# Optimization experiments

Hardware: AMD Instinct MI355X
Metric: run time of the kernel (lower is better)

## Reference

```python
import jax, jax.numpy as jnp
import numpy as np

E, H = 512, 8
D = E // H  # head_dim = 64
NEG = jnp.finfo(jnp.float32).min


def setup_inputs() -> dict:
    key = jax.random.key(0)
    ks = jax.random.split(key, 12)
    s = 0.02
    return {
        "image": jax.random.normal(ks[0], (16, 197, E), jnp.float32),
        "text": jax.random.normal(ks[1], (64, 30, E), jnp.float32),
        "text_mask": jax.random.randint(ks[2], (64, 29), 0, 2).astype(bool),
        "Wq": jax.random.normal(ks[3], (D, D), jnp.float32) * s,
        "Wk": jax.random.normal(ks[4], (D, D), jnp.float32) * s,
        "Wv": jax.random.normal(ks[5], (D, D), jnp.float32) * s,
        "W_out": jax.random.normal(ks[6], (E, E), jnp.float32) * s,
        "b_out": jnp.zeros((E,), jnp.float32),
        "Wtv": jax.random.normal(ks[7], (D, D), jnp.float32) * s,
        "W_out_text": jax.random.normal(ks[8], (E, E), jnp.float32) * s,
        "b_out_text": jnp.zeros((E,), jnp.float32),
    }


def reference(image, text, text_mask, Wq, Wk, Wv, W_out, b_out, Wtv, W_out_text, b_out_text):
    I, Q, _ = image.shape
    T, K, _ = text.shape
    img = image.reshape(I, Q, H, D)
    txt = text.reshape(T, K, H, D)
    # per-head linear projections (torch Linear: y = x @ W.T)
    q = img @ Wq.T            # [I,Q,H,D]
    k = txt @ Wk.T            # [T,K,H,D]
    v = txt @ Wv.T            # [T,K,H,D]
    # cross-batch bidirectional attention energy [I,T,H,Q,K]
    energy = jnp.einsum('tkhd,iqhd->ithqk', k, q)
    # cls_present: pad mask with True at front along K
    mask = jnp.pad(text_mask, ((0, 0), (1, 0)), constant_values=True)  # [T,K]
    energy = jnp.where(mask[None, :, None, None, :], energy, NEG)
    scaled = energy / jnp.sqrt(jnp.float32(E))
    attention = jax.nn.softmax(scaled, axis=-1)       # over k (i2t)
    text_attention = jax.nn.softmax(scaled, axis=-2)  # over q (t2i)
    # i2t branch: [I,T,Q,H,D] -> [I,T,Q,E]
    out = jnp.einsum('ithqk,tkhd->itqhd', attention, v).reshape(I, T, Q, E)
    out = out @ W_out.T + b_out
    out = out.mean(axis=2)  # mean pool over image tokens -> [I,T,E]
    # t2i branch: [I,T,K,H,D] -> [I,T,K,E]
    tv = img @ Wtv.T  # [I,Q,H,D]
    out_text = jnp.einsum('ithqk,iqhd->itkhd', text_attention, tv).reshape(I, T, K, E)
    out_text = out_text @ W_out_text.T + b_out_text
    out_text = out_text.mean(axis=2)  # mean pool over text tokens -> [I,T,E]
    return (out, out_text, attention, text_attention)
```

## Files before the change

kernel.cpp:

```cpp
#include <hip/hip_runtime.h>
#include <hip/hip_bf16.h>
#include <cstdint>

#define I_ 16
#define T_ 64
#define Q_ 197
#define K_ 30
#define H_ 8
#define D_ 64
#define E_ 512

typedef float f32x2 __attribute__((ext_vector_type(2)));
typedef float f32x4 __attribute__((ext_vector_type(4)));
typedef short bf16x8 __attribute__((ext_vector_type(8)));

static constexpr float INV_SQRT_E = 0.044194173824159216f;
static constexpr float C197 = 1.0f / 197.0f;
static constexpr int   QK = Q_ * K_;

#define OFF_QBF   0
#define OFF_KBF   806912
#define OFF_VBF   1298432
#define OFF_TVBF  1789952
#define OFF_ASUM  2596864
#define OFF_TASUM 2842624
#define OFF_PBF   4456448
#define OFF_WBF   4980736

__global__ __launch_bounds__(512) void proj_kernel(
    const float* __restrict__ image, const float* __restrict__ text,
    const float* __restrict__ Wq, const float* __restrict__ Wk,
    const float* __restrict__ Wv, const float* __restrict__ Wtv,
    const float* __restrict__ W_out, const float* __restrict__ W_out_text,
    float* __restrict__ ws)
{
  const int NQ4 = (I_ * Q_) / 4;
  const int NT4 = (T_ * K_) / 4;
  int bb = blockIdx.x;
  int tid = threadIdx.x;

  if (bb >= NQ4 + 2 * NT4 + NQ4) {
    int row0 = (bb - (NQ4 + 2 * NT4 + NQ4)) * 4;
    __hip_bfloat16* Wb = (__hip_bfloat16*)(ws + OFF_WBF);
    const float* src = (row0 < 512) ? (W_out + row0 * E_) : (W_out_text + (row0 - 512) * E_);
    #pragma unroll
    for (int rr = 0; rr < 4; ++rr)
      Wb[(size_t)(row0 + rr) * E_ + tid] = __float2bfloat16(src[rr * E_ + tid]);
    return;
  }

  const float* X; const float* W; int row0; int mode;
  if (bb < NQ4)             { X = image; W = Wq;  row0 = bb * 4;               mode = 0; }
  else if (bb < NQ4 + NT4)  { X = text;  W = Wk;  row0 = (bb - NQ4) * 4;       mode = 1; }
  else if (bb < NQ4 + 2*NT4){ X = text;  W = Wv;  row0 = (bb - NQ4 - NT4) * 4; mode = 2; }
  else                      { X = image; W = Wtv; row0 = (bb - NQ4 - 2*NT4)*4; mode = 3; }

  __shared__ float s_x[4][E_];
  __shared__ float s_w[D_][D_ + 1];
  for (int idx = tid; idx < D_ * D_; idx += 512) s_w[idx >> 6][idx & 63] = W[idx];
  #pragma unroll
  for (int rr = 0; rr < 4; ++rr) s_x[rr][tid] = X[(size_t)(row0 + rr) * E_ + tid];
  __syncthreads();

  int h = tid >> 6, dout = tid & 63;
  float a0 = 0.f, a1 = 0.f, a2 = 0.f, a3 = 0.f;
  #pragma unroll
  for (int d = 0; d < D_; ++d) {
    float w = s_w[dout][d];
    a0 = fmaf(s_x[0][h * 64 + d], w, a0);
    a1 = fmaf(s_x[1][h * 64 + d], w, a1);
    a2 = fmaf(s_x[2][h * 64 + d], w, a2);
    a3 = fmaf(s_x[3][h * 64 + d], w, a3);
  }
  static const int offs[4] = { OFF_QBF, OFF_KBF, OFF_VBF, OFF_TVBF };
  __hip_bfloat16* Y = (__hip_bfloat16*)(ws + offs[mode]);
  Y[(size_t)(row0 + 0) * E_ + tid] = __float2bfloat16(a0);
  Y[(size_t)(row0 + 1) * E_ + tid] = __float2bfloat16(a1);
  Y[(size_t)(row0 + 2) * E_ + tid] = __float2bfloat16(a2);
  Y[(size_t)(row0 + 3) * E_ + tid] = __float2bfloat16(a3);
}

__global__ __launch_bounds__(256, 8) void attn_kernel(
    const __hip_bfloat16* __restrict__ qbf, const __hip_bfloat16* __restrict__ kbf,
    const int* __restrict__ text_mask,
    float* __restrict__ attn_out, float* __restrict__ tattn_out,
    float* __restrict__ A_sum, float* __restrict__ TA_sum)
{
  int b = blockIdx.x;
  int h = b & 7, t = (b >> 3) & 63, i = b >> 9;
  int tid = threadIdx.x;
  int w = tid >> 6, lane = tid & 63;
  int lr = lane & 15, lg = lane >> 4;

  __shared__ __hip_bfloat16 s_e[208 * 30];
  __shared__ float s_invrow[208];
  __shared__ float s_cd[4][32];
  __shared__ float s_ca[4][32];
  __shared__ float s_invd[32];
  __shared__ int   s_mask[32];

  if (tid < 32) s_mask[tid] = (tid == 0) ? 1 : (tid < K_ ? text_mask[t * (K_ - 1) + tid - 1] : 0);

  int m0 = (lr == 0) ? 1 : text_mask[t * (K_ - 1) + lr - 1];
  int m1 = (lr < 14) ? text_mask[t * (K_ - 1) + 15 + lr] : 0;

  const __hip_bfloat16* qb = qbf + ((size_t)(i * Q_) * H_ + h) * D_;
  const __hip_bfloat16* kb = kbf + ((size_t)(t * K_) * H_ + h) * D_;

  const bf16x8* bp0 = (const bf16x8*)(kb + (size_t)lr * (H_ * D_) + lg * 8);
  const bf16x8* bp1 = (const bf16x8*)(kb + (size_t)(16 + lr) * (H_ * D_) + lg * 8);
  bf16x8 b00 = bp0[0], b01 = bp0[4];
  bf16x8 b10 = bp1[0], b11 = bp1[4];

  float cd0 = 0.f, cd1 = 0.f, ca0 = 0.f, ca1 = 0.f;

  #pragma unroll
  for (int j = 0; j < 4; ++j) {
    int mt = w + 4 * j;
    if (mt < 13) {
      const bf16x8* ap = (const bf16x8*)(qb + (size_t)(mt * 16 + lr) * (H_ * D_) + lg * 8);
      bf16x8 a0 = ap[0], a1 = ap[4];
      f32x4 acc0 = {0.f, 0.f, 0.f, 0.f}, acc1 = {0.f, 0.f, 0.f, 0.f};
      acc0 = __builtin_amdgcn_mfma_f32_16x16x32_bf16(a0, b00, acc0, 0, 0, 0);
      acc0 = __builtin_amdgcn_mfma_f32_16x16x32_bf16(a1, b01, acc0, 0, 0, 0);
      acc1 = __builtin_amdgcn_mfma_f32_16x16x32_bf16(a0, b10, acc1, 0, 0, 0);
      acc1 = __builtin_amdgcn_mfma_f32_16x16x32_bf16(a1, b11, acc1, 0, 0, 0);
      int row0 = mt * 16 + lg * 4;
      float v0[4], v1[4];
      #pragma unroll
      for (int r = 0; r < 4; ++r) {
        bool vr = (row0 + r) < Q_;
        v0[r] = (vr && m0) ? __expf(acc0[r] * INV_SQRT_E) : 0.f;
        v1[r] = (vr && m1) ? __expf(acc1[r] * INV_SQRT_E) : 0.f;
        s_e[(row0 + r) * K_ + lr] = __float2bfloat16(v0[r]);
        if (lr < 14) s_e[(row0 + r) * K_ + 16 + lr] = __float2bfloat16(v1[r]);
      }
      #pragma unroll
      for (int r = 0; r < 4; ++r) {
        float s = v0[r] + v1[r];
        s += __shfl_xor(s, 1);
        s += __shfl_xor(s, 2);
        s += __shfl_xor(s, 4);
        s += __shfl_xor(s, 8);
        float iv = ((row0 + r) < Q_ && s > 0.f) ? (1.0f / s) : 0.f;
        if (lr == 0) s_invrow[row0 + r] = iv;
        cd0 += v0[r]; ca0 += v0[r] * iv;
        cd1 += v1[r]; ca1 += v1[r] * iv;
      }
    }
  }

  cd0 += __shfl_xor(cd0, 16); cd0 += __shfl_xor(cd0, 32);
  ca0 += __shfl_xor(ca0, 16); ca0 += __shfl_xor(ca0, 32);
  cd1 += __shfl_xor(cd1, 16); cd1 += __shfl_xor(cd1, 32);
  ca1 += __shfl_xor(ca1, 16); ca1 += __shfl_xor(ca1, 32);
  if (lane < 16) {
    s_cd[w][lr] = cd0; s_cd[w][lr + 16] = cd1;
    s_ca[w][lr] = ca0; s_ca[w][lr + 16] = ca1;
  }
  __syncthreads();

  if (tid < 32) {
    int col = tid;
    float d  = s_cd[0][col] + s_cd[1][col] + s_cd[2][col] + s_cd[3][col];
    float pa = s_ca[0][col] + s_ca[1][col] + s_ca[2][col] + s_ca[3][col];
    s_invd[col] = (s_mask[col] && d > 0.f) ? (1.0f / d) : 0.f;
    if (col < K_) A_sum[(size_t)b * K_ + col] = pa;
  }
  __syncthreads();

  if (tid < Q_) {
    float ta = 0.f;
    #pragma unroll
    for (int kk = 0; kk < K_; ++kk) {
      float ev = __bfloat162float(s_e[tid * K_ + kk]);
      ta += s_mask[kk] ? ev * s_invd[kk] : C197;
    }
    TA_sum[(size_t)b * Q_ + tid] = ta;
  }

  {
    float* abase = attn_out  + (size_t)b * QK;
    float* tbase = tattn_out + (size_t)b * QK;
    int head = (b & 1) ? 2 : 0;
    if (tid == 0) {
      int e0 = head ? 0 : (QK - 2);
      float ex = __bfloat162float(s_e[e0]);
      float ey = __bfloat162float(s_e[e0 + 1]);
      int r0 = e0 / K_, c0 = e0 - r0 * K_;
      int r1 = (e0 + 1) / K_, c1 = (e0 + 1) - r1 * K_;
      f32x2 av = { ex * s_invrow[r0], ey * s_invrow[r1] };
      f32x2 tv2 = { s_mask[c0] ? ex * s_invd[c0] : C197,
                    s_mask[c1] ? ey * s_invd[c1] : C197 };
      *(f32x2*)(abase + e0) = av;
      *(f32x2*)(tbase + e0) = tv2;
    }
    for (int fi = tid; fi < 1477; fi += 256) {
      int base = head + fi * 4;
      float ev[4]; int rw[4]; int cl[4];
      #pragma unroll
      for (int e = 0; e < 4; ++e) {
        int idx = base + e;
        ev[e] = __bfloat162float(s_e[idx]);
        rw[e] = idx / K_;
        cl[e] = idx - rw[e] * K_;
      }
      f32x4 av, tv4;
      #pragma unroll
      for (int e = 0; e < 4; ++e) {
        av[e]  = ev[e] * s_invrow[rw[e]];
        tv4[e] = s_mask[cl[e]] ? ev[e] * s_invd[cl[e]] : C197;
      }
      *(f32x4*)(abase + base) = av;
      *(f32x4*)(tbase + base) = tv4;
    }
  }
}

__global__ __launch_bounds__(512) void pool_fused_kernel(
    const float* __restrict__ A_sum, const float* __restrict__ TA_sum,
    const __hip_bfloat16* __restrict__ vbf, const __hip_bfloat16* __restrict__ tvbf,
    __hip_bfloat16* __restrict__ Pbf)
{
  int bt = blockIdx.x;
  int t = bt & 63;
  int i = bt >> 6;
  int tid = threadIdx.x;
  int h = tid >> 6, d = tid & 63;
  __shared__ float s_A[H_ * K_];
  __shared__ float s_TA[H_ * Q_];
  if (tid < H_ * K_) s_A[tid] = A_sum[(size_t)bt * H_ * K_ + tid];
  for (int idx = tid; idx < H_ * Q_; idx += 512) s_TA[idx] = TA_sum[(size_t)bt * H_ * Q_ + idx];
  __syncthreads();

  {
    float a0 = 0.f, a1 = 0.f;
    #pragma unroll
    for (int kk = 0; kk < K_; kk += 2) {
      a0 = fmaf(s_A[h * K_ + kk],
                __bfloat162float(vbf[((size_t)(t * K_ + kk)     * H_ + h) * D_ + d]), a0);
      a1 = fmaf(s_A[h * K_ + kk + 1],
                __bfloat162float(vbf[((size_t)(t * K_ + kk + 1) * H_ + h) * D_ + d]), a1);
    }
    Pbf[(size_t)bt * E_ + tid] = __float2bfloat16((a0 + a1) * C197);
  }

  {
    float a0 = 0.f, a1 = 0.f, a2 = 0.f, a3 = 0.f;
    int qq = 0;
    for (; qq + 4 <= Q_; qq += 4) {
      a0 = fmaf(s_TA[h * Q_ + qq + 0],
                __bfloat162float(tvbf[((size_t)(i * Q_ + qq + 0) * H_ + h) * D_ + d]), a0);
      a1 = fmaf(s_TA[h * Q_ + qq + 1],
                __bfloat162float(tvbf[((size_t)(i * Q_ + qq + 1) * H_ + h) * D_ + d]), a1);
      a2 = fmaf(s_TA[h * Q_ + qq + 2],
                __bfloat162float(tvbf[((size_t)(i * Q_ + qq + 2) * H_ + h) * D_ + d]), a2);
      a3 = fmaf(s_TA[h * Q_ + qq + 3],
                __bfloat162float(tvbf[((size_t)(i * Q_ + qq + 3) * H_ + h) * D_ + d]), a3);
    }
    for (; qq < Q_; ++qq)
      a0 = fmaf(s_TA[h * Q_ + qq],
                __bfloat162float(tvbf[((size_t)(i * Q_ + qq) * H_ + h) * D_ + d]), a0);
    Pbf[(size_t)(1024 + bt) * E_ + tid] = __float2bfloat16(((a0 + a1) + (a2 + a3)) * (1.0f / 30.0f));
  }
}

__global__ __launch_bounds__(256) void outproj_mfma_kernel(
    const __hip_bfloat16* __restrict__ Pbf, const __hip_bfloat16* __restrict__ Wbf,
    const float* __restrict__ b_out, const float* __restrict__ b_out_text,
    float* __restrict__ out)
{
  int mt = blockIdx.x;
  int z = (mt >= 64);
  int tid = threadIdx.x;
  int w = tid >> 6, lane = tid & 63;
  int lr = lane & 15, lg = lane >> 4;

  const __hip_bfloat16* A = Pbf + (size_t)(mt * 16 + lr) * E_ + lg * 8;
  const __hip_bfloat16* B = Wbf + (size_t)(z * 512) * E_;
  f32x4 acc[8] = {};
  for (int ks = 0; ks < 16; ++ks) {
    bf16x8 a = *(const bf16x8*)(A + ks * 32);
    #pragma unroll
    for (int nt = 0; nt < 8; ++nt) {
      int n0 = w * 128 + nt * 16;
      bf16x8 bv = *(const bf16x8*)(B + (size_t)(n0 + lr) * E_ + ks * 32 + lg * 8);
      acc[nt] = __builtin_amdgcn_mfma_f32_16x16x32_bf16(a, bv, acc[nt], 0, 0, 0);
    }
  }
  const float* bias = z ? b_out_text : b_out;
  int row0 = mt * 16 + lg * 4;
  #pragma unroll
  for (int nt = 0; nt < 8; ++nt) {
    int n = w * 128 + nt * 16 + lr;
    float bv = bias[n];
    #pragma unroll
    for (int r = 0; r < 4; ++r)
      out[(size_t)(row0 + r) * E_ + n] = acc[nt][r] + bv;
  }
}

extern "C" void kernel_launch(void* const* d_in, const int* in_sizes, int n_in,
                              void* d_out, int out_size, void* d_ws, size_t ws_size,
                              hipStream_t stream)
{
  const float* image      = (const float*)d_in[0];
  const float* text       = (const float*)d_in[1];
  const int*   tmask      = (const int*)d_in[2];
  const float* Wq         = (const float*)d_in[3];
  const float* Wk         = (const float*)d_in[4];
  const float* Wv         = (const float*)d_in[5];
  const float* W_out      = (const float*)d_in[6];
  const float* b_out      = (const float*)d_in[7];
  const float* Wtv        = (const float*)d_in[8];
  const float* W_out_text = (const float*)d_in[9];
  const float* b_out_text = (const float*)d_in[10];

  float* out = (float*)d_out;
  float* ws  = (float*)d_ws;

  const __hip_bfloat16* qbf  = (const __hip_bfloat16*)(ws + OFF_QBF);
  const __hip_bfloat16* kbf  = (const __hip_bfloat16*)(ws + OFF_KBF);
  const __hip_bfloat16* vbf  = (const __hip_bfloat16*)(ws + OFF_VBF);
  const __hip_bfloat16* tvbf = (const __hip_bfloat16*)(ws + OFF_TVBF);
  float* Asum  = ws + OFF_ASUM;
  float* TAsum = ws + OFF_TASUM;
  __hip_bfloat16* Pbf = (__hip_bfloat16*)(ws + OFF_PBF);
  __hip_bfloat16* Wbf = (__hip_bfloat16*)(ws + OFF_WBF);

  float* attn    = out + (size_t)2 * I_ * T_ * E_;
  float* tattn   = attn + (size_t)I_ * T_ * H_ * Q_ * K_;

  const int NQ4 = (I_ * Q_) / 4, NT4 = (T_ * K_) / 4;
  proj_kernel<<<NQ4 + 2 * NT4 + NQ4 + 256, 512, 0, stream>>>(
      image, text, Wq, Wk, Wv, Wtv, W_out, W_out_text, ws);
  attn_kernel<<<I_ * T_ * H_, 256, 0, stream>>>(qbf, kbf, tmask, attn, tattn, Asum, TAsum);
  pool_fused_kernel<<<I_ * T_, 512, 0, stream>>>(Asum, TAsum, vbf, tvbf, Pbf);
  outproj_mfma_kernel<<<128, 256, 0, stream>>>(Pbf, Wbf, b_out, b_out_text, out);
}
```

Baseline: 192.7 us.

## Map one (i,t,h) attention tile per wavefront and keep exponentials in registers

The attention kernel now assigns each wavefront a whole (i,t,h) problem instead of splitting the 13 query tiles across a block's four waves. The exponentials stay packed in registers, and the column denominators and per-row t2i sums are reduced with shuffles, so the block-level syncs and the shared bf16 energy buffer are no longer needed. Outputs are staged per query tile in small per-wave shared buffers and written as coalesced float2 stores. The cost is higher register pressure from the 13 packed vectors, with launch bounds lowered to 4 blocks, and each wave carries a longer serial loop.

Result: slower. 269.3 us (+39.7%).

```diff
diff --git a/kernel.cpp b/kernel.cpp
--- a/kernel.cpp
+++ b/kernel.cpp
@@ -27,6 +27,9 @@
 #define OFF_PBF   4456448
 #define OFF_WBF   4980736
 
+__device__ inline short f2bs(float x) { __hip_bfloat16 h = __float2bfloat16(x); return *reinterpret_cast<short*>(&h); }
+__device__ inline float bs2f(short s) { __hip_bfloat16 h = *reinterpret_cast<__hip_bfloat16*>(&s); return __bfloat162float(h); }
+
 __global__ __launch_bounds__(512) void proj_kernel(
     const float* __restrict__ image, const float* __restrict__ text,
     const float* __restrict__ Wq, const float* __restrict__ Wk,
@@ -80,26 +83,21 @@
   Y[(size_t)(row0 + 3) * E_ + tid] = __float2bfloat16(a3);
 }
 
-__global__ __launch_bounds__(256, 8) void attn_kernel(
+__global__ __launch_bounds__(256, 4) void attn_kernel(
     const __hip_bfloat16* __restrict__ qbf, const __hip_bfloat16* __restrict__ kbf,
     const int* __restrict__ text_mask,
     float* __restrict__ attn_out, float* __restrict__ tattn_out,
     float* __restrict__ A_sum, float* __restrict__ TA_sum)
 {
-  int b = blockIdx.x;
-  int h = b & 7, t = (b >> 3) & 63, i = b >> 9;
   int tid = threadIdx.x;
   int w = tid >> 6, lane = tid & 63;
   int lr = lane & 15, lg = lane >> 4;
-
-  __shared__ __hip_bfloat16 s_e[208 * 30];
-  __shared__ float s_invrow[208];
-  __shared__ float s_cd[4][32];
-  __shared__ float s_ca[4][32];
-  __shared__ float s_invd[32];
-  __shared__ int   s_mask[32];
-
-  if (tid < 32) s_mask[tid] = (tid == 0) ? 1 : (tid < K_ ? text_mask[t * (K_ - 1) + tid - 1] : 0);
+  int b = blockIdx.x * 4 + w;
+  int h = b & 7, t = (b >> 3) & 63, i = b >> 9;
+
+  __shared__ __align__(16) float s_ivr[4][208];
+  __shared__ __align__(16) float s_av[4][480];
+  __shared__ __align__(16) float s_tv[4][480];
 
   int m0 = (lr == 0) ? 1 : text_mask[t * (K_ - 1) + lr - 1];
   int m1 = (lr < 14) ? text_mask[t * (K_ - 1) + 15 + lr] : 0;
@@ -113,106 +111,101 @@
   bf16x8 b10 = bp1[0], b11 = bp1[4];
 
   float cd0 = 0.f, cd1 = 0.f, ca0 = 0.f, ca1 = 0.f;
-
-  #pragma unroll
-  for (int j = 0; j < 4; ++j) {
-    int mt = w + 4 * j;
-    if (mt < 13) {
-      const bf16x8* ap = (const bf16x8*)(qb + (size_t)(mt * 16 + lr) * (H_ * D_) + lg * 8);
-      bf16x8 a0 = ap[0], a1 = ap[4];
-      f32x4 acc0 = {0.f, 0.f, 0.f, 0.f}, acc1 = {0.f, 0.f, 0.f, 0.f};
-      acc0 = __builtin_amdgcn_mfma_f32_16x16x32_bf16(a0, b00, acc0, 0, 0, 0);
-      acc0 = __builtin_amdgcn_mfma_f32_16x16x32_bf16(a1, b01, acc0, 0, 0, 0);
-      acc1 = __builtin_amdgcn_mfma_f32_16x16x32_bf16(a0, b10, acc1, 0, 0, 0);
-      acc1 = __builtin_amdgcn_mfma_f32_16x16x32_bf16(a1, b11, acc1, 0, 0, 0);
-      int row0 = mt * 16 + lg * 4;
-      float v0[4], v1[4];
+  bf16x8 epk[13];
+
+  #pragma unroll
+  for (int qt = 0; qt < 13; ++qt) {
+    const bf16x8* ap = (const bf16x8*)(qb + (size_t)(qt * 16 + lr) * (H_ * D_) + lg * 8);
+    bf16x8 a0 = ap[0], a1 = ap[4];
+    f32x4 acc0 = {0.f, 0.f, 0.f, 0.f}, acc1 = {0.f, 0.f, 0.f, 0.f};
+    acc0 = __builtin_amdgcn_mfma_f32_16x16x32_bf16(a0, b00, acc0, 0, 0, 0);
+    acc0 = __builtin_amdgcn_mfma_f32_16x16x32_bf16(a1, b01, acc0, 0, 0, 0);
+    acc1 = __builtin_amdgcn_mfma_f32_16x16x32_bf16(a0, b10, acc1, 0, 0, 0);
+    acc1 = __builtin_amdgcn_mfma_f32_16x16x32_bf16(a1, b11, acc1, 0, 0, 0);
+    int row0 = qt * 16 + lg * 4;
+    float v0[4], v1[4], iv[4];
+    #pragma unroll
+    for (int r = 0; r < 4; ++r) {
+      bool vr = (row0 + r) < Q_;
+      v0[r] = (vr && m0) ? __expf(acc0[r] * INV_SQRT_E) : 0.f;
+      v1[r] = (vr && m1) ? __expf(acc1[r] * INV_SQRT_E) : 0.f;
+    }
+    #pragma unroll
+    for (int r = 0; r < 4; ++r) {
+      float s = v0[r] + v1[r];
+      s += __shfl_xor(s, 1);
+      s += __shfl_xor(s, 2);
+      s += __shfl_xor(s, 4);
+      s += __shfl_xor(s, 8);
+      iv[r] = ((row0 + r) < Q_ && s > 0.f) ? (1.0f / s) : 0.f;
+      cd0 += v0[r]; ca0 += v0[r] * iv[r];
+      cd1 += v1[r]; ca1 += v1[r] * iv[r];
+    }
+    if (lr == 0) {
       #pragma unroll
-      for (int r = 0; r < 4; ++r) {
-        bool vr = (row0 + r) < Q_;
-        v0[r] = (vr && m0) ? __expf(acc0[r] * INV_SQRT_E) : 0.f;
-        v1[r] = (vr && m1) ? __expf(acc1[r] * INV_SQRT_E) : 0.f;
-        s_e[(row0 + r) * K_ + lr] = __float2bfloat16(v0[r]);
-        if (lr < 14) s_e[(row0 + r) * K_ + 16 + lr] = __float2bfloat16(v1[r]);
+      for (int r = 0; r < 4; ++r) s_ivr[w][row0 + r] = iv[r];
+    }
+    epk[qt] = bf16x8{ f2bs(v0[0]), f2bs(v0[1]), f2bs(v0[2]), f2bs(v0[3]),
+                      f2bs(v1[0]), f2bs(v1[1]), f2bs(v1[2]), f2bs(v1[3]) };
+  }
+
+  cd0 += __shfl_xor(cd0, 16); cd0 += __shfl_xor(cd0, 32);
+  cd1 += __shfl_xor(cd1, 16); cd1 += __shfl_xor(cd1, 32);
+  ca0 += __shfl_xor(ca0, 16); ca0 += __shfl_xor(ca0, 32);
+  ca1 += __shfl_xor(ca1, 16); ca1 += __shfl_xor(ca1, 32);
+
+  float invd0 = (m0 && cd0 > 0.f) ? (1.0f / cd0) : 0.f;
+  float invd1 = (m1 && cd1 > 0.f) ? (1.0f / cd1) : 0.f;
+
+  if (lane < 16) {
+    A_sum[(size_t)b * K_ + lr] = ca0;
+    if (lr < 14) A_sum[(size_t)b * K_ + 16 + lr] = ca1;
+  }
+
+  float* abase   = attn_out  + (size_t)b * QK;
+  float* tbase   = tattn_out + (size_t)b * QK;
+  float* ta_base = TA_sum    + (size_t)b * Q_;
+
+  #pragma unroll
+  for (int qt = 0; qt < 13; ++qt) {
+    int row0 = qt * 16 + lg * 4;
+    f32x4 iv4 = *(const f32x4*)&s_ivr[w][qt * 16 + lg * 4];
+    float tvA[4], tvB[4];
+    #pragma unroll
+    for (int r = 0; r < 4; ++r) {
+      float eA = bs2f(epk[qt][r]);
+      float eB = bs2f(epk[qt][4 + r]);
+      float avA = eA * iv4[r];
+      float avB = eB * iv4[r];
+      tvA[r] = m0 ? eA * invd0 : C197;
+      tvB[r] = m1 ? eB * invd1 : C197;
+      int rl = lg * 4 + r;
+      s_av[w][rl * K_ + lr] = avA;
+      s_tv[w][rl * K_ + lr] = tvA[r];
+      if (lr < 14) {
+        s_av[w][rl * K_ + 16 + lr] = avB;
+        s_tv[w][rl * K_ + 16 + lr] = tvB[r];
       }
-      #pragma unroll
-      for (int r = 0; r < 4; ++r) {
-        float s = v0[r] + v1[r];
-        s += __shfl_xor(s, 1);
-        s += __shfl_xor(s, 2);
-        s += __shfl_xor(s, 4);
-        s += __shfl_xor(s, 8);
-        float iv = ((row0 + r) < Q_ && s > 0.f) ? (1.0f / s) : 0.f;
-        if (lr == 0) s_invrow[row0 + r] = iv;
-        cd0 += v0[r]; ca0 += v0[r] * iv;
-        cd1 += v1[r]; ca1 += v1[r] * iv;
+    }
+    #pragma unroll
+    for (int r = 0; r < 4; ++r) {
+      float ta = tvA[r] + ((lr < 14) ? tvB[r] : 0.f);
+      ta += __shfl_xor(ta, 1);
+      ta += __shfl_xor(ta, 2);
+      ta += __shfl_xor(ta, 4);
+      ta += __shfl_xor(ta, 8);
+      if (lr == 0 && (row0 + r) < Q_) ta_base[row0 + r] = ta;
+    }
+    const int nstore = (qt < 12) ? 240 : 75;
+    #pragma unroll
+    for (int it = 0; it < 4; ++it) {
+      int idx = it * 64 + lane;
+      if (idx < nstore) {
+        f32x2 a2 = *(const f32x2*)&s_av[w][2 * idx];
+        f32x2 t2 = *(const f32x2*)&s_tv[w][2 * idx];
+        *(f32x2*)(abase + qt * 480 + 2 * idx) = a2;
+        *(f32x2*)(tbase + qt * 480 + 2 * idx) = t2;
       }
-    }
-  }
-
-  cd0 += __shfl_xor(cd0, 16); cd0 += __shfl_xor(cd0, 32);
-  ca0 += __shfl_xor(ca0, 16); ca0 += __shfl_xor(ca0, 32);
-  cd1 += __shfl_xor(cd1, 16); cd1 += __shfl_xor(cd1, 32);
-  ca1 += __shfl_xor(ca1, 16); ca1 += __shfl_xor(ca1, 32);
-  if (lane < 16) {
-    s_cd[w][lr] = cd0; s_cd[w][lr + 16] = cd1;
-    s_ca[w][lr] = ca0; s_ca[w][lr + 16] = ca1;
-  }
-  __syncthreads();
-
-  if (tid < 32) {
-    int col = tid;
-    float d  = s_cd[0][col] + s_cd[1][col] + s_cd[2][col] + s_cd[3][col];
-    float pa = s_ca[0][col] + s_ca[1][col] + s_ca[2][col] + s_ca[3][col];
-    s_invd[col] = (s_mask[col] && d > 0.f) ? (1.0f / d) : 0.f;
-    if (col < K_) A_sum[(size_t)b * K_ + col] = pa;
-  }
-  __syncthreads();
-
-  if (tid < Q_) {
-    float ta = 0.f;
-    #pragma unroll
-    for (int kk = 0; kk < K_; ++kk) {
-      float ev = __bfloat162float(s_e[tid * K_ + kk]);
-      ta += s_mask[kk] ? ev * s_invd[kk] : C197;
-    }
-    TA_sum[(size_t)b * Q_ + tid] = ta;
-  }
-
-  {
-    float* abase = attn_out  + (size_t)b * QK;
-    float* tbase = tattn_out + (size_t)b * QK;
-    int head = (b & 1) ? 2 : 0;
-    if (tid == 0) {
-      int e0 = head ? 0 : (QK - 2);
-      float ex = __bfloat162float(s_e[e0]);
-      float ey = __bfloat162float(s_e[e0 + 1]);
-      int r0 = e0 / K_, c0 = e0 - r0 * K_;
-      int r1 = (e0 + 1) / K_, c1 = (e0 + 1) - r1 * K_;
-      f32x2 av = { ex * s_invrow[r0], ey * s_invrow[r1] };
-      f32x2 tv2 = { s_mask[c0] ? ex * s_invd[c0] : C197,
-                    s_mask[c1] ? ey * s_invd[c1] : C197 };
-      *(f32x2*)(abase + e0) = av;
-      *(f32x2*)(tbase + e0) = tv2;
-    }
-    for (int fi = tid; fi < 1477; fi += 256) {
-      int base = head + fi * 4;
-      float ev[4]; int rw[4]; int cl[4];
-      #pragma unroll
-      for (int e = 0; e < 4; ++e) {
-        int idx = base + e;
-        ev[e] = __bfloat162float(s_e[idx]);
-        rw[e] = idx / K_;
-        cl[e] = idx - rw[e] * K_;
-      }
-      f32x4 av, tv4;
-      #pragma unroll
-      for (int e = 0; e < 4; ++e) {
-        av[e]  = ev[e] * s_invrow[rw[e]];
-        tv4[e] = s_mask[cl[e]] ? ev[e] * s_invd[cl[e]] : C197;
-      }
-      *(f32x4*)(abase + base) = av;
-      *(f32x4*)(tbase + base) = tv4;
     }
   }
 }
@@ -334,7 +327,7 @@
   const int NQ4 = (I_ * Q_) / 4, NT4 = (T_ * K_) / 4;
   proj_kernel<<<NQ4 + 2 * NT4 + NQ4 + 256, 512, 0, stream>>>(
       image, text, Wq, Wk, Wv, Wtv, W_out, W_out_text, ws);
-  attn_kernel<<<I_ * T_ * H_, 256, 0, stream>>>(qbf, kbf, tmask, attn, tattn, Asum, TAsum);
+  attn_kernel<<<(I_ * T_ * H_) / 4, 256, 0, stream>>>(qbf, kbf, tmask, attn, tattn, Asum, TAsum);
   pool_fused_kernel<<<I_ * T_, 512, 0, stream>>>(Asum, TAsum, vbf, tvbf, Pbf);
   outproj_mfma_kernel<<<128, 256, 0, stream>>>(Pbf, Wbf, b_out, b_out_text, out);
 }
```
